# Performance work log

Hardware: AMD Instinct MI355X
Metric: run time of the kernel (lower is better)

Reference implementation:

```python
import jax, jax.numpy as jnp
import numpy as np

B, C, H, W = 4, 128, 64, 64
NUM_HEADS = 4
EPS = 1e-5


def setup_inputs() -> dict:
    key = jax.random.key(0)
    k1, k2, k3 = jax.random.split(key, 3)
    x = jax.random.normal(k1, (B, C, H, W), dtype=jnp.float32)
    gn_w = jnp.ones((C,), jnp.float32)
    gn_b = jnp.zeros((C,), jnp.float32)
    qkv_w = 0.02 * jax.random.normal(k2, (3 * C, C), dtype=jnp.float32)
    qkv_b = jnp.zeros((3 * C,), jnp.float32)
    proj_w = 0.02 * jax.random.normal(k3, (C, C), dtype=jnp.float32)
    proj_b = jnp.zeros((C,), jnp.float32)
    return {"x": x, "gn_w": gn_w, "gn_b": gn_b, "qkv_w": qkv_w,
            "qkv_b": qkv_b, "proj_w": proj_w, "proj_b": proj_b}


def reference(x, gn_w, gn_b, qkv_w, qkv_b, proj_w, proj_b):
    b, c, h, w = x.shape
    nh = NUM_HEADS
    dh = c // nh
    hw = h * w
    # GroupNorm with 1 group: normalize over (C,H,W) per sample, biased var
    mean = jnp.mean(x, axis=(1, 2, 3), keepdims=True)
    var = jnp.var(x, axis=(1, 2, 3), keepdims=True)
    xn = (x - mean) * jax.lax.rsqrt(var + EPS)
    xn = xn * gn_w[None, :, None, None] + gn_b[None, :, None, None]
    # 1x1 conv == channel matmul: (b,c,h,w) -> (b,3c,h,w)
    qkv = jnp.einsum('bchw,oc->bohw', xn, qkv_w) + qkv_b[None, :, None, None]
    qkv = qkv.reshape(b, 3, nh, dh, hw)
    q, k, v = qkv[:, 0], qkv[:, 1], qkv[:, 2]  # each (b, nh, dh, hw)
    scale = dh ** (-0.5)
    # attn: (b, nh, hw, hw)
    attn = jax.nn.softmax(jnp.einsum('bhdn,bhdm->bhnm', q, k) * scale, axis=-1)
    out = jnp.einsum('bhnm,bhdm->bhnd', attn, v)  # (b, nh, hw, dh)
    # faithful to torch: permute(0,3,1,2) -> (b, dh, nh, hw), then reshape(b,c,h,w)
    out = jnp.transpose(out, (0, 3, 1, 2)).reshape(b, c, h, w)
    out = jnp.einsum('bchw,oc->bohw', out, proj_w) + proj_b[None, :, None, None]
    return out + x
```

## Files before the change

### kernel.cpp

```cpp
#include <hip/hip_runtime.h>
#include <math.h>

#define HW 4096
#define CH 128
#define NH 4
#define DH 32

typedef unsigned short u16;
typedef __attribute__((ext_vector_type(8))) short bf16x8;
typedef __attribute__((ext_vector_type(4))) float f32x4;
typedef __attribute__((ext_vector_type(16))) float f32x16;
typedef __attribute__((ext_vector_type(4))) unsigned short u16x4;
typedef __attribute__((ext_vector_type(8))) unsigned short u16x8;

#if __has_builtin(__builtin_amdgcn_exp2f)
#define KFOLD (0.17677669529663687f * 1.4426950408889634f)
#define FASTEXP(x) __builtin_amdgcn_exp2f(x)
#else
#define KFOLD 0.17677669529663687f
#define FASTEXP(x) __expf(x)
#endif

#if __has_builtin(__builtin_amdgcn_rcpf)
#define RCPF(x) __builtin_amdgcn_rcpf(x)
#else
#define RCPF(x) (1.f / (x))
#endif

__device__ __forceinline__ u16 f2bf(float f) {
    union { float f; unsigned u; } a; a.f = f;
    unsigned u = a.u;
    unsigned r = u + 0x7FFFu + ((u >> 16) & 1u);
    return (u16)(r >> 16);
}
__device__ __forceinline__ float bf2f(u16 u) {
    union { unsigned u; float f; } a; a.u = ((unsigned)u) << 16;
    return a.f;
}
__device__ __forceinline__ unsigned pack2bf_t(float a, float b) {
    union { float f; unsigned u; } ua, ub; ua.f = a; ub.f = b;
    return __builtin_amdgcn_perm(ub.u, ua.u, 0x07060302u);
}

__global__ __launch_bounds__(256) void prep_kernel(
    const float* __restrict__ x, float* __restrict__ partials,
    const float* __restrict__ qkv_w, const float* __restrict__ proj_w,
    u16* __restrict__ wq, u16* __restrict__ wp) {
    int blk = blockIdx.x, t = threadIdx.x;
    if (blk < 512) {
        const float4* xv = (const float4*)(x + (size_t)blk * 4096);
        float s = 0.f, sq = 0.f;
#pragma unroll
        for (int i = 0; i < 4; ++i) {
            float4 v = xv[t + 256 * i];
            s  += v.x + v.y + v.z + v.w;
            sq += v.x * v.x + v.y * v.y + v.z * v.z + v.w * v.w;
        }
#pragma unroll
        for (int off = 32; off > 0; off >>= 1) {
            s  += __shfl_down(s, off, 64);
            sq += __shfl_down(sq, off, 64);
        }
        __shared__ float red[8];
        int wave = t >> 6, lane = t & 63;
        if (lane == 0) { red[wave * 2] = s; red[wave * 2 + 1] = sq; }
        __syncthreads();
        if (t == 0) {
            partials[blk * 2]     = red[0] + red[2] + red[4] + red[6];
            partials[blk * 2 + 1] = red[1] + red[3] + red[5] + red[7];
        }
    } else {
        int i = (blk - 512) * 256 + t;
        if (i < 49152) {
            int dstBlk = i >> 9, lane = (i >> 3) & 63, j = i & 7;
            int wave = dstBlk / 24, rem = dstBlk % 24;
            int os = rem >> 2, kc = rem & 3;
            int o = wave * 96 + os * 16 + (lane & 15);
            int c = kc * 32 + (lane >> 4) * 8 + j;
            wq[i] = f2bf(qkv_w[o * 128 + c]);
        } else {
            int i2 = i - 49152;
            int dstBlk = i2 >> 9, lane = (i2 >> 3) & 63, j = i2 & 7;
            int wave = dstBlk >> 3, rem = dstBlk & 7;
            int os = rem >> 2, kc = rem & 3;
            int o = wave * 32 + os * 16 + (lane & 15);
            int c = kc * 32 + (lane >> 4) * 8 + j;
            wp[i2] = f2bf(proj_w[o * 128 + c]);
        }
    }
}

__global__ __launch_bounds__(256) void qkv_mfma_kernel(
    const float* __restrict__ x, const float* __restrict__ gn_w, const float* __restrict__ gn_b,
    const u16* __restrict__ wq, const float* __restrict__ qkv_b, const float* __restrict__ partials,
    u16* __restrict__ qo, u16* __restrict__ ko, u16* __restrict__ vo) {
    __shared__ u16 xt[32 * 136];
    __shared__ float sstats[2];
    int b = blockIdx.y, p0 = blockIdx.x * 32, t = threadIdx.x;
    const float* xb = x + (size_t)b * CH * HW;
    float4 xv[4]; int cc[4], pp[4];
#pragma unroll
    for (int i = 0; i < 4; ++i) {
        int u = t + 256 * i;
        cc[i] = u >> 3; pp[i] = (u & 7) * 4;
        xv[i] = *(const float4*)&xb[(size_t)cc[i] * HW + p0 + pp[i]];
    }
    if (t < 64) {
        float s  = partials[(b * 128 + t) * 2]     + partials[(b * 128 + 64 + t) * 2];
        float sq = partials[(b * 128 + t) * 2 + 1] + partials[(b * 128 + 64 + t) * 2 + 1];
#pragma unroll
        for (int off = 32; off > 0; off >>= 1) {
            s  += __shfl_down(s, off, 64);
            sq += __shfl_down(sq, off, 64);
        }
        if (t == 0) {
            const float invN = 1.f / (float)(CH * HW);
            float mean = s * invN;
            float var  = sq * invN - mean * mean;
            sstats[0] = mean;
            sstats[1] = rsqrtf(var + 1e-5f);
        }
    }
    __syncthreads();
    float mean = sstats[0], rstd = sstats[1];
#pragma unroll
    for (int i = 0; i < 4; ++i) {
        float sc = rstd * gn_w[cc[i]], bb = gn_b[cc[i]] - mean * sc;
        xt[(pp[i] + 0) * 136 + cc[i]] = f2bf(fmaf(xv[i].x, sc, bb));
        xt[(pp[i] + 1) * 136 + cc[i]] = f2bf(fmaf(xv[i].y, sc, bb));
        xt[(pp[i] + 2) * 136 + cc[i]] = f2bf(fmaf(xv[i].z, sc, bb));
        xt[(pp[i] + 3) * 136 + cc[i]] = f2bf(fmaf(xv[i].w, sc, bb));
    }
    __syncthreads();
    int wave = t >> 6, lane = t & 63, l16 = lane & 15, quad = lane >> 4;
    f32x4 acc[6][2];
#pragma unroll
    for (int os = 0; os < 6; ++os)
#pragma unroll
        for (int ps = 0; ps < 2; ++ps) acc[os][ps] = f32x4{0.f, 0.f, 0.f, 0.f};
#pragma unroll
    for (int kc = 0; kc < 4; ++kc) {
        bf16x8 bfr[2];
#pragma unroll
        for (int ps = 0; ps < 2; ++ps)
            bfr[ps] = *(const bf16x8*)&xt[(ps * 16 + l16) * 136 + kc * 32 + quad * 8];
#pragma unroll
        for (int os = 0; os < 6; ++os) {
            bf16x8 af = *(const bf16x8*)&wq[((wave * 6 + os) * 4 + kc) * 512 + lane * 8];
#pragma unroll
            for (int ps = 0; ps < 2; ++ps)
                acc[os][ps] = __builtin_amdgcn_mfma_f32_16x16x32_bf16(af, bfr[ps], acc[os][ps], 0, 0, 0);
        }
    }
#pragma unroll
    for (int os = 0; os < 6; ++os) {
        int obase = wave * 96 + os * 16 + quad * 4;
        int sec = obase >> 7;
        if (sec == 2) continue;
        float4 bias = *(const float4*)&qkv_b[obase];
        int oc = obase & 127, h = oc >> 5, d = oc & 31;
        float km = (sec == 1) ? KFOLD : 1.f;
#pragma unroll
        for (int ps = 0; ps < 2; ++ps) {
            int p = p0 + ps * 16 + l16;
            u16x4 pk = {f2bf((acc[os][ps][0] + bias.x) * km),
                        f2bf((acc[os][ps][1] + bias.y) * km),
                        f2bf((acc[os][ps][2] + bias.z) * km),
                        f2bf((acc[os][ps][3] + bias.w) * km)};
            *(u16x4*)((sec == 0 ? qo : ko) + ((size_t)(b * NH + h) * HW + p) * DH + d) = pk;
        }
    }
    __syncthreads();
    u16* vt = xt;
    int l16p2 = (l16 & 3) | ((l16 & 4) << 1) | ((l16 & 8) >> 1);
#pragma unroll
    for (int os = 0; os < 6; ++os) {
        int obase = wave * 96 + os * 16 + quad * 4;
        if ((obase >> 7) != 2) continue;
        float4 bias = *(const float4*)&qkv_b[obase];
        int oc = obase & 127;
#pragma unroll
        for (int ps = 0; ps < 2; ++ps) {
            int colm = ps * 16 + l16p2;
            vt[(oc + 0) * 34 + colm] = f2bf(acc[os][ps][0] + bias.x);
            vt[(oc + 1) * 34 + colm] = f2bf(acc[os][ps][1] + bias.y);
            vt[(oc + 2) * 34 + colm] = f2bf(acc[os][ps][2] + bias.z);
            vt[(oc + 3) * 34 + colm] = f2bf(acc[os][ps][3] + bias.w);
        }
    }
    __syncthreads();
#pragma unroll
    for (int i = 0; i < 2; ++i) {
        int row = i * 64 + (t >> 2), colv = (t & 3) * 8;
        *(u16x8*)&vo[((size_t)b * CH + row) * HW + p0 + colv] = *(const u16x8*)&vt[row * 34 + colv];
    }
}

__global__ __launch_bounds__(256, 4) void attn_mfma_kernel(
    const u16* __restrict__ q, const u16* __restrict__ k, const u16* __restrict__ v,
    u16* __restrict__ Op, float* __restrict__ lp) {
    __shared__ u16 smem[18944];
    int bh = blockIdx.z, mpart = blockIdx.y, t = threadIdx.x;
    int wave = t >> 6, lane = t & 63, l31 = lane & 31, hf = lane >> 5;
    const u16* qb = q + (size_t)bh * HW * DH;
    const u16* kb = k + (size_t)bh * HW * DH;
    const u16* vb = v + (size_t)bh * DH * HW;
    int n_g = blockIdx.x * 128 + wave * 32 + l31;
    int m_base = mpart * 2048;

    bf16x8 bq0 = *(const bf16x8*)&qb[(size_t)n_g * DH + hf * 8];
    bf16x8 bq1 = *(const bf16x8*)&qb[(size_t)n_g * DH + 16 + hf * 8];

    int km_ = t >> 2, kg_ = t & 3;
    int kw0 = km_ * 40 + kg_ * 8, kw1 = kw0 + 64 * 40;
    const u16* kgp = kb + (size_t)(m_base + km_) * DH + kg_ * 8;
    int vd_ = t >> 3, vg_ = t & 7;
    int vw0 = vd_ * 136 + vg_ * 8, vw1 = vw0 + 64;
    const u16* vgp = vb + (size_t)vd_ * HW + m_base + vg_ * 8;

    int kro[2][2], vro[4];
#pragma unroll
    for (int ms = 0; ms < 2; ++ms)
#pragma unroll
        for (int kc = 0; kc < 2; ++kc)
            kro[ms][kc] = (ms * 32 + l31) * 40 + (2 * kc + hf) * 8;
#pragma unroll
    for (int kc = 0; kc < 4; ++kc)
        vro[kc] = l31 * 136 + (2 * kc + hf) * 8;

    const f32x16 zero16 = {0.f,0.f,0.f,0.f,0.f,0.f,0.f,0.f,0.f,0.f,0.f,0.f,0.f,0.f,0.f,0.f};
    f32x16 accO = zero16;
    float l_part = 0.f;

    bf16x8 kregA = *(const bf16x8*)kgp;
    bf16x8 kregB = *(const bf16x8*)(kgp + 64 * DH);
    bf16x8 vregA = *(const bf16x8*)vgp;
    bf16x8 vregB = *(const bf16x8*)(vgp + 64);

    for (int it = 0; it < 16; ++it) {
        u16* Ksb = smem + (it & 1) * 5120;
        u16* Vsb = smem + 10240 + (it & 1) * 4352;
        *(bf16x8*)&Ksb[kw0] = kregA;
        *(bf16x8*)&Ksb[kw1] = kregB;
        *(bf16x8*)&Vsb[vw0] = vregA;
        *(bf16x8*)&Vsb[vw1] = vregB;
        __syncthreads();
        if (it < 15) {
            const u16* kp = kgp + (size_t)(it + 1) * 128 * DH;
            kregA = *(const bf16x8*)kp;
            kregB = *(const bf16x8*)(kp + 64 * DH);
            const u16* vp = vgp + (it + 1) * 128;
            vregA = *(const bf16x8*)vp;
            vregB = *(const bf16x8*)(vp + 64);
        }
#pragma unroll
        for (int h = 0; h < 2; ++h) {
            const u16* Kh = Ksb + h * 2560;
            f32x16 s0, s1;
            {
                bf16x8 a00 = *(const bf16x8*)&Kh[kro[0][0]];
                bf16x8 a01 = *(const bf16x8*)&Kh[kro[0][1]];
                s0 = __builtin_amdgcn_mfma_f32_32x32x16_bf16(a00, bq0, zero16, 0, 0, 0);
                s0 = __builtin_amdgcn_mfma_f32_32x32x16_bf16(a01, bq1, s0, 0, 0, 0);
                bf16x8 a10 = *(const bf16x8*)&Kh[kro[1][0]];
                bf16x8 a11 = *(const bf16x8*)&Kh[kro[1][1]];
                s1 = __builtin_amdgcn_mfma_f32_32x32x16_bf16(a10, bq0, zero16, 0, 0, 0);
                s1 = __builtin_amdgcn_mfma_f32_32x32x16_bf16(a11, bq1, s1, 0, 0, 0);
            }
            unsigned pk[2][8];
#pragma unroll
            for (int qq = 0; qq < 8; ++qq) {
                float e0 = FASTEXP(s0[2 * qq]), e1 = FASTEXP(s0[2 * qq + 1]);
                l_part += e0 + e1;
                pk[0][qq] = pack2bf_t(e0, e1);
                float f0 = FASTEXP(s1[2 * qq]), f1 = FASTEXP(s1[2 * qq + 1]);
                l_part += f0 + f1;
                pk[1][qq] = pack2bf_t(f0, f1);
            }
#pragma unroll
            for (int kc = 0; kc < 4; ++kc) {
                int ms = kc >> 1, Qb = 4 * (kc & 1);
                union { unsigned u[4]; bf16x8 v; } bu;
                bu.u[0] = pk[ms][Qb + 0];
                bu.u[1] = pk[ms][Qb + 1];
                bu.u[2] = pk[ms][Qb + 2];
                bu.u[3] = pk[ms][Qb + 3];
                bf16x8 av = *(const bf16x8*)&Vsb[vro[kc] + h * 64];
                accO = __builtin_amdgcn_mfma_f32_32x32x16_bf16(av, bu.v, accO, 0, 0, 0);
            }
        }
    }
    l_part += __shfl_xor(l_part, 32, 64);
    if (hf == 0) lp[((size_t)bh * HW + n_g) * 2 + mpart] = l_part;
    __syncthreads();
    u16* tb = smem;
    int nloc = wave * 32 + l31;
#pragma unroll
    for (int r = 0; r < 16; ++r) {
        int d = (r & 3) + 8 * (r >> 2) + 4 * hf;
        tb[nloc * 40 + d] = f2bf(accO[r]);
    }
    __syncthreads();
    size_t obase = ((size_t)(mpart * 16 + bh) * HW + blockIdx.x * 128) * 32;
#pragma unroll
    for (int i = 0; i < 2; ++i) {
        int row = i * 64 + (t >> 2), col = (t & 3) * 8;
        *(u16x8*)&Op[obase + (size_t)row * 32 + col] = *(const u16x8*)&tb[row * 40 + col];
    }
}

__global__ __launch_bounds__(256) void proj_mfma_kernel(
    const u16* __restrict__ Op, const float* __restrict__ lp,
    const u16* __restrict__ wp, const float* __restrict__ proj_b,
    const float* __restrict__ x, float* __restrict__ out) {
    __shared__ u16 at_t[32 * 136];
    int b = blockIdx.y, p0 = blockIdx.x * 32, t = threadIdx.x;
#pragma unroll
    for (int i = 0; i < 2; ++i) {
        int u = t + 256 * i;
        int p = u >> 4, hh = (u >> 2) & 3, ch = u & 3;
        int bh = b * NH + hh;
        size_t nidx = (size_t)bh * HW + p0 + p;
        float2 l2 = *(const float2*)&lp[nidx * 2];
        float lsum = l2.x + l2.y;
        float sum8[8] = {0.f,0.f,0.f,0.f,0.f,0.f,0.f,0.f};
#pragma unroll
        for (int part = 0; part < 2; ++part) {
            u16x8 ov = *(const u16x8*)&Op[((size_t)(part * 16 + bh) * HW + p0 + p) * 32 + ch * 8];
#pragma unroll
            for (int j = 0; j < 8; ++j) sum8[j] += bf2f(ov[j]);
        }
        float rin = RCPF(lsum);
#pragma unroll
        for (int j = 0; j < 8; ++j)
            at_t[p * 136 + (ch * 8 + j) * 4 + hh] = f2bf(sum8[j] * rin);
    }
    __syncthreads();
    int wave = t >> 6, lane = t & 63, l16 = lane & 15, quad = lane >> 4;
    f32x4 acc[2][2];
#pragma unroll
    for (int os = 0; os < 2; ++os)
#pragma unroll
        for (int ps = 0; ps < 2; ++ps) acc[os][ps] = f32x4{0.f, 0.f, 0.f, 0.f};
#pragma unroll
    for (int kc = 0; kc < 4; ++kc) {
        bf16x8 bfr[2];
#pragma unroll
        for (int ps = 0; ps < 2; ++ps)
            bfr[ps] = *(const bf16x8*)&at_t[(ps * 16 + l16) * 136 + kc * 32 + quad * 8];
#pragma unroll
        for (int os = 0; os < 2; ++os) {
            bf16x8 af = *(const bf16x8*)&wp[((wave * 2 + os) * 4 + kc) * 512 + lane * 8];
#pragma unroll
            for (int ps = 0; ps < 2; ++ps)
                acc[os][ps] = __builtin_amdgcn_mfma_f32_16x16x32_bf16(af, bfr[ps], acc[os][ps], 0, 0, 0);
        }
    }
#pragma unroll
    for (int os = 0; os < 2; ++os) {
        int obase = wave * 32 + os * 16 + quad * 4;
#pragma unroll
        for (int ps = 0; ps < 2; ++ps) {
            int p = p0 + ps * 16 + l16;
#pragma unroll
            for (int r = 0; r < 4; ++r) {
                size_t idx = ((size_t)b * CH + obase + r) * HW + p;
                out[idx] = acc[os][ps][r] + proj_b[obase + r] + x[idx];
            }
        }
    }
}

extern "C" void kernel_launch(void* const* d_in, const int* in_sizes, int n_in,
                              void* d_out, int out_size, void* d_ws, size_t ws_size,
                              hipStream_t stream) {
    const float* x      = (const float*)d_in[0];
    const float* gn_w   = (const float*)d_in[1];
    const float* gn_b   = (const float*)d_in[2];
    const float* qkv_w  = (const float*)d_in[3];
    const float* qkv_b  = (const float*)d_in[4];
    const float* proj_w = (const float*)d_in[5];
    const float* proj_b = (const float*)d_in[6];
    float* out = (float*)d_out;

    char* W = (char*)d_ws;
    float* partials = (float*)(W + 0);
    u16*   wq       = (u16*)(W + 8192);
    u16*   wp       = (u16*)(W + 8192 + 98304);
    u16*   qo       = (u16*)(W + 139264);
    u16*   ko       = qo + (size_t)2097152;
    u16*   vo       = ko + (size_t)2097152;
    u16*   Op       = vo + (size_t)2097152;
    float* lp       = (float*)(Op + (size_t)2 * 2097152);

    hipLaunchKernelGGL(prep_kernel,      dim3(768),       dim3(256), 0, stream,
                       x, partials, qkv_w, proj_w, wq, wp);
    hipLaunchKernelGGL(qkv_mfma_kernel,  dim3(128, 4),    dim3(256), 0, stream,
                       x, gn_w, gn_b, wq, qkv_b, partials, qo, ko, vo);
    hipLaunchKernelGGL(attn_mfma_kernel, dim3(32, 2, 16), dim3(256), 0, stream,
                       qo, ko, vo, Op, lp);
    hipLaunchKernelGGL(proj_mfma_kernel, dim3(128, 4),    dim3(256), 0, stream,
                       Op, lp, wp, proj_b, x, out);
}
```

Measured before the change: 137.4 us.

## Halve pixel tile in qkv/proj kernels and split attention accumulator chain

The qkv and proj kernels now process 16 pixels per block instead of 32, doubling the grid to 1024 blocks so more work spreads across CUs, at the cost of reloading weights from global memory twice as often. The attention kernel splits its PV accumulator into two independent MFMA chains (and two row-sum partials), combined at the end, to cut the dependency stall between back-to-back 32x32 MFMAs. The extra accumulator adds 16 registers per lane, which may pressure occupancy under the launch bound of 4.

```diff
diff --git a/kernel.cpp b/kernel.cpp
--- a/kernel.cpp
+++ b/kernel.cpp
@@ -94,15 +94,15 @@
     const float* __restrict__ x, const float* __restrict__ gn_w, const float* __restrict__ gn_b,
     const u16* __restrict__ wq, const float* __restrict__ qkv_b, const float* __restrict__ partials,
     u16* __restrict__ qo, u16* __restrict__ ko, u16* __restrict__ vo) {
-    __shared__ u16 xt[32 * 136];
+    __shared__ u16 smem[3072];
     __shared__ float sstats[2];
-    int b = blockIdx.y, p0 = blockIdx.x * 32, t = threadIdx.x;
+    int b = blockIdx.y, p0 = blockIdx.x * 16, t = threadIdx.x;
     const float* xb = x + (size_t)b * CH * HW;
-    float4 xv[4]; int cc[4], pp[4];
-#pragma unroll
-    for (int i = 0; i < 4; ++i) {
+    float4 xv[2]; int cc[2], pp[2];
+#pragma unroll
+    for (int i = 0; i < 2; ++i) {
         int u = t + 256 * i;
-        cc[i] = u >> 3; pp[i] = (u & 7) * 4;
+        cc[i] = u >> 2; pp[i] = (u & 3) * 4;
         xv[i] = *(const float4*)&xb[(size_t)cc[i] * HW + p0 + pp[i]];
     }
     if (t < 64) {
@@ -123,8 +123,9 @@
     }
     __syncthreads();
     float mean = sstats[0], rstd = sstats[1];
-#pragma unroll
-    for (int i = 0; i < 4; ++i) {
+    u16* xt = smem;
+#pragma unroll
+    for (int i = 0; i < 2; ++i) {
         float sc = rstd * gn_w[cc[i]], bb = gn_b[cc[i]] - mean * sc;
         xt[(pp[i] + 0) * 136 + cc[i]] = f2bf(fmaf(xv[i].x, sc, bb));
         xt[(pp[i] + 1) * 136 + cc[i]] = f2bf(fmaf(xv[i].y, sc, bb));
@@ -133,25 +134,19 @@
     }
     __syncthreads();
     int wave = t >> 6, lane = t & 63, l16 = lane & 15, quad = lane >> 4;
-    f32x4 acc[6][2];
-#pragma unroll
-    for (int os = 0; os < 6; ++os)
-#pragma unroll
-        for (int ps = 0; ps < 2; ++ps) acc[os][ps] = f32x4{0.f, 0.f, 0.f, 0.f};
+    f32x4 acc[6];
+#pragma unroll
+    for (int os = 0; os < 6; ++os) acc[os] = f32x4{0.f, 0.f, 0.f, 0.f};
 #pragma unroll
     for (int kc = 0; kc < 4; ++kc) {
-        bf16x8 bfr[2];
-#pragma unroll
-        for (int ps = 0; ps < 2; ++ps)
-            bfr[ps] = *(const bf16x8*)&xt[(ps * 16 + l16) * 136 + kc * 32 + quad * 8];
+        bf16x8 bfr = *(const bf16x8*)&xt[l16 * 136 + kc * 32 + quad * 8];
 #pragma unroll
         for (int os = 0; os < 6; ++os) {
             bf16x8 af = *(const bf16x8*)&wq[((wave * 6 + os) * 4 + kc) * 512 + lane * 8];
-#pragma unroll
-            for (int ps = 0; ps < 2; ++ps)
-                acc[os][ps] = __builtin_amdgcn_mfma_f32_16x16x32_bf16(af, bfr[ps], acc[os][ps], 0, 0, 0);
-        }
-    }
+            acc[os] = __builtin_amdgcn_mfma_f32_16x16x32_bf16(af, bfr, acc[os], 0, 0, 0);
+        }
+    }
+    int p = p0 + l16;
 #pragma unroll
     for (int os = 0; os < 6; ++os) {
         int obase = wave * 96 + os * 16 + quad * 4;
@@ -160,18 +155,14 @@
         float4 bias = *(const float4*)&qkv_b[obase];
         int oc = obase & 127, h = oc >> 5, d = oc & 31;
         float km = (sec == 1) ? KFOLD : 1.f;
-#pragma unroll
-        for (int ps = 0; ps < 2; ++ps) {
-            int p = p0 + ps * 16 + l16;
-            u16x4 pk = {f2bf((acc[os][ps][0] + bias.x) * km),
-                        f2bf((acc[os][ps][1] + bias.y) * km),
-                        f2bf((acc[os][ps][2] + bias.z) * km),
-                        f2bf((acc[os][ps][3] + bias.w) * km)};
-            *(u16x4*)((sec == 0 ? qo : ko) + ((size_t)(b * NH + h) * HW + p) * DH + d) = pk;
-        }
-    }
-    __syncthreads();
-    u16* vt = xt;
+        u16x4 pk = {f2bf((acc[os][0] + bias.x) * km),
+                    f2bf((acc[os][1] + bias.y) * km),
+                    f2bf((acc[os][2] + bias.z) * km),
+                    f2bf((acc[os][3] + bias.w) * km)};
+        *(u16x4*)((sec == 0 ? qo : ko) + ((size_t)(b * NH + h) * HW + p) * DH + d) = pk;
+    }
+    __syncthreads();
+    u16* vt = smem;
     int l16p2 = (l16 & 3) | ((l16 & 4) << 1) | ((l16 & 8) >> 1);
 #pragma unroll
     for (int os = 0; os < 6; ++os) {
@@ -179,20 +170,15 @@
         if ((obase >> 7) != 2) continue;
         float4 bias = *(const float4*)&qkv_b[obase];
         int oc = obase & 127;
-#pragma unroll
-        for (int ps = 0; ps < 2; ++ps) {
-            int colm = ps * 16 + l16p2;
-            vt[(oc + 0) * 34 + colm] = f2bf(acc[os][ps][0] + bias.x);
-            vt[(oc + 1) * 34 + colm] = f2bf(acc[os][ps][1] + bias.y);
-            vt[(oc + 2) * 34 + colm] = f2bf(acc[os][ps][2] + bias.z);
-            vt[(oc + 3) * 34 + colm] = f2bf(acc[os][ps][3] + bias.w);
-        }
-    }
-    __syncthreads();
-#pragma unroll
-    for (int i = 0; i < 2; ++i) {
-        int row = i * 64 + (t >> 2), colv = (t & 3) * 8;
-        *(u16x8*)&vo[((size_t)b * CH + row) * HW + p0 + colv] = *(const u16x8*)&vt[row * 34 + colv];
+        vt[(oc + 0) * 24 + l16p2] = f2bf(acc[os][0] + bias.x);
+        vt[(oc + 1) * 24 + l16p2] = f2bf(acc[os][1] + bias.y);
+        vt[(oc + 2) * 24 + l16p2] = f2bf(acc[os][2] + bias.z);
+        vt[(oc + 3) * 24 + l16p2] = f2bf(acc[os][3] + bias.w);
+    }
+    __syncthreads();
+    {
+        int row = t >> 1, col = (t & 1) * 8;
+        *(u16x8*)&vo[((size_t)b * CH + row) * HW + p0 + col] = *(const u16x8*)&vt[row * 24 + col];
     }
 }
 
@@ -229,8 +215,8 @@
         vro[kc] = l31 * 136 + (2 * kc + hf) * 8;
 
     const f32x16 zero16 = {0.f,0.f,0.f,0.f,0.f,0.f,0.f,0.f,0.f,0.f,0.f,0.f,0.f,0.f,0.f,0.f};
-    f32x16 accO = zero16;
-    float l_part = 0.f;
+    f32x16 accO0 = zero16, accO1 = zero16;
+    float l0 = 0.f, l1 = 0.f;
 
     bf16x8 kregA = *(const bf16x8*)kgp;
     bf16x8 kregB = *(const bf16x8*)(kgp + 64 * DH);
@@ -271,10 +257,10 @@
 #pragma unroll
             for (int qq = 0; qq < 8; ++qq) {
                 float e0 = FASTEXP(s0[2 * qq]), e1 = FASTEXP(s0[2 * qq + 1]);
-                l_part += e0 + e1;
+                l0 += e0 + e1;
                 pk[0][qq] = pack2bf_t(e0, e1);
                 float f0 = FASTEXP(s1[2 * qq]), f1 = FASTEXP(s1[2 * qq + 1]);
-                l_part += f0 + f1;
+                l1 += f0 + f1;
                 pk[1][qq] = pack2bf_t(f0, f1);
             }
 #pragma unroll
@@ -286,10 +272,15 @@
                 bu.u[2] = pk[ms][Qb + 2];
                 bu.u[3] = pk[ms][Qb + 3];
                 bf16x8 av = *(const bf16x8*)&Vsb[vro[kc] + h * 64];
-                accO = __builtin_amdgcn_mfma_f32_32x32x16_bf16(av, bu.v, accO, 0, 0, 0);
+                if (kc < 2)
+                    accO0 = __builtin_amdgcn_mfma_f32_32x32x16_bf16(av, bu.v, accO0, 0, 0, 0);
+                else
+                    accO1 = __builtin_amdgcn_mfma_f32_32x32x16_bf16(av, bu.v, accO1, 0, 0, 0);
             }
         }
     }
+    f32x16 accO = accO0 + accO1;
+    float l_part = l0 + l1;
     l_part += __shfl_xor(l_part, 32, 64);
     if (hf == 0) lp[((size_t)bh * HW + n_g) * 2 + mpart] = l_part;
     __syncthreads();
@@ -313,12 +304,10 @@
     const u16* __restrict__ Op, const float* __restrict__ lp,
     const u16* __restrict__ wp, const float* __restrict__ proj_b,
     const float* __restrict__ x, float* __restrict__ out) {
-    __shared__ u16 at_t[32 * 136];
-    int b = blockIdx.y, p0 = blockIdx.x * 32, t = threadIdx.x;
-#pragma unroll
-    for (int i = 0; i < 2; ++i) {
-        int u = t + 256 * i;
-        int p = u >> 4, hh = (u >> 2) & 3, ch = u & 3;
+    __shared__ u16 at_t[16 * 136];
+    int b = blockIdx.y, p0 = blockIdx.x * 16, t = threadIdx.x;
+    {
+        int p = t >> 4, hh = (t >> 2) & 3, ch = t & 3;
         int bh = b * NH + hh;
         size_t nidx = (size_t)bh * HW + p0 + p;
         float2 l2 = *(const float2*)&lp[nidx * 2];
@@ -337,36 +326,26 @@
     }
     __syncthreads();
     int wave = t >> 6, lane = t & 63, l16 = lane & 15, quad = lane >> 4;
-    f32x4 acc[2][2];
-#pragma unroll
-    for (int os = 0; os < 2; ++os)
-#pragma unroll
-        for (int ps = 0; ps < 2; ++ps) acc[os][ps] = f32x4{0.f, 0.f, 0.f, 0.f};
+    f32x4 acc[2];
+    acc[0] = f32x4{0.f, 0.f, 0.f, 0.f};
+    acc[1] = f32x4{0.f, 0.f, 0.f, 0.f};
 #pragma unroll
     for (int kc = 0; kc < 4; ++kc) {
-        bf16x8 bfr[2];
-#pragma unroll
-        for (int ps = 0; ps < 2; ++ps)
-            bfr[ps] = *(const bf16x8*)&at_t[(ps * 16 + l16) * 136 + kc * 32 + quad * 8];
+        bf16x8 bfr = *(const bf16x8*)&at_t[l16 * 136 + kc * 32 + quad * 8];
 #pragma unroll
         for (int os = 0; os < 2; ++os) {
             bf16x8 af = *(const bf16x8*)&wp[((wave * 2 + os) * 4 + kc) * 512 + lane * 8];
-#pragma unroll
-            for (int ps = 0; ps < 2; ++ps)
-                acc[os][ps] = __builtin_amdgcn_mfma_f32_16x16x32_bf16(af, bfr[ps], acc[os][ps], 0, 0, 0);
-        }
-    }
+            acc[os] = __builtin_amdgcn_mfma_f32_16x16x32_bf16(af, bfr, acc[os], 0, 0, 0);
+        }
+    }
+    int p = p0 + l16;
 #pragma unroll
     for (int os = 0; os < 2; ++os) {
         int obase = wave * 32 + os * 16 + quad * 4;
 #pragma unroll
-        for (int ps = 0; ps < 2; ++ps) {
-            int p = p0 + ps * 16 + l16;
-#pragma unroll
-            for (int r = 0; r < 4; ++r) {
-                size_t idx = ((size_t)b * CH + obase + r) * HW + p;
-                out[idx] = acc[os][ps][r] + proj_b[obase + r] + x[idx];
-            }
+        for (int r = 0; r < 4; ++r) {
+            size_t idx = ((size_t)b * CH + obase + r) * HW + p;
+            out[idx] = acc[os][r] + proj_b[obase + r] + x[idx];
         }
     }
 }
@@ -395,10 +374,10 @@
 
     hipLaunchKernelGGL(prep_kernel,      dim3(768),       dim3(256), 0, stream,
                        x, partials, qkv_w, proj_w, wq, wp);
-    hipLaunchKernelGGL(qkv_mfma_kernel,  dim3(128, 4),    dim3(256), 0, stream,
+    hipLaunchKernelGGL(qkv_mfma_kernel,  dim3(256, 4),    dim3(256), 0, stream,
                        x, gn_w, gn_b, wq, qkv_b, partials, qo, ko, vo);
     hipLaunchKernelGGL(attn_mfma_kernel, dim3(32, 2, 16), dim3(256), 0, stream,
                        qo, ko, vo, Op, lp);
-    hipLaunchKernelGGL(proj_mfma_kernel, dim3(128, 4),    dim3(256), 0, stream,
+    hipLaunchKernelGGL(proj_mfma_kernel, dim3(256, 4),    dim3(256), 0, stream,
                        Op, lp, wp, proj_b, x, out);
 }
```

Result: slower. 148.2 us (+7.9%).

## Process two query tiles per wave to reuse K/V loads, split keys four ways

Applied to the files above, without the earlier changes.

Each attention block now handles 256 queries (two 32-row sub-tiles per wave) and reuses each K/V fragment read from shared memory for both, which halves K/V global and LDS traffic per query. The key dimension is split into four parts of 1024 instead of two of 2048, which keeps the grid size unchanged. The projection kernel now reduces four partial outputs and four partial sums per query. The cost is more registers (two accumulators, two sets of Q fragments, with the occupancy hint removed) and extra partial-output memory and reduction work in the projection step.

```diff
diff --git a/kernel.cpp b/kernel.cpp
--- a/kernel.cpp
+++ b/kernel.cpp
@@ -196,7 +196,7 @@
     }
 }
 
-__global__ __launch_bounds__(256, 4) void attn_mfma_kernel(
+__global__ __launch_bounds__(256) void attn_mfma_kernel(
     const u16* __restrict__ q, const u16* __restrict__ k, const u16* __restrict__ v,
     u16* __restrict__ Op, float* __restrict__ lp) {
     __shared__ u16 smem[18944];
@@ -205,11 +205,15 @@
     const u16* qb = q + (size_t)bh * HW * DH;
     const u16* kb = k + (size_t)bh * HW * DH;
     const u16* vb = v + (size_t)bh * DH * HW;
-    int n_g = blockIdx.x * 128 + wave * 32 + l31;
-    int m_base = mpart * 2048;
-
-    bf16x8 bq0 = *(const bf16x8*)&qb[(size_t)n_g * DH + hf * 8];
-    bf16x8 bq1 = *(const bf16x8*)&qb[(size_t)n_g * DH + 16 + hf * 8];
+    int n_base = blockIdx.x * 256 + wave * 32 + l31;
+    int m_base = mpart * 1024;
+
+    bf16x8 bq0[2], bq1[2];
+#pragma unroll
+    for (int s = 0; s < 2; ++s) {
+        bq0[s] = *(const bf16x8*)&qb[(size_t)(n_base + s * 128) * DH + hf * 8];
+        bq1[s] = *(const bf16x8*)&qb[(size_t)(n_base + s * 128) * DH + 16 + hf * 8];
+    }
 
     int km_ = t >> 2, kg_ = t & 3;
     int kw0 = km_ * 40 + kg_ * 8, kw1 = kw0 + 64 * 40;
@@ -229,15 +233,16 @@
         vro[kc] = l31 * 136 + (2 * kc + hf) * 8;
 
     const f32x16 zero16 = {0.f,0.f,0.f,0.f,0.f,0.f,0.f,0.f,0.f,0.f,0.f,0.f,0.f,0.f,0.f,0.f};
-    f32x16 accO = zero16;
-    float l_part = 0.f;
+    f32x16 accO[2];
+    accO[0] = zero16; accO[1] = zero16;
+    float lprt[2] = {0.f, 0.f};
 
     bf16x8 kregA = *(const bf16x8*)kgp;
     bf16x8 kregB = *(const bf16x8*)(kgp + 64 * DH);
     bf16x8 vregA = *(const bf16x8*)vgp;
     bf16x8 vregB = *(const bf16x8*)(vgp + 64);
 
-    for (int it = 0; it < 16; ++it) {
+    for (int it = 0; it < 8; ++it) {
         u16* Ksb = smem + (it & 1) * 5120;
         u16* Vsb = smem + 10240 + (it & 1) * 4352;
         *(bf16x8*)&Ksb[kw0] = kregA;
@@ -245,7 +250,7 @@
         *(bf16x8*)&Vsb[vw0] = vregA;
         *(bf16x8*)&Vsb[vw1] = vregB;
         __syncthreads();
-        if (it < 15) {
+        if (it < 7) {
             const u16* kp = kgp + (size_t)(it + 1) * 128 * DH;
             kregA = *(const bf16x8*)kp;
             kregB = *(const bf16x8*)(kp + 64 * DH);
@@ -256,54 +261,70 @@
 #pragma unroll
         for (int h = 0; h < 2; ++h) {
             const u16* Kh = Ksb + h * 2560;
-            f32x16 s0, s1;
-            {
-                bf16x8 a00 = *(const bf16x8*)&Kh[kro[0][0]];
-                bf16x8 a01 = *(const bf16x8*)&Kh[kro[0][1]];
-                s0 = __builtin_amdgcn_mfma_f32_32x32x16_bf16(a00, bq0, zero16, 0, 0, 0);
-                s0 = __builtin_amdgcn_mfma_f32_32x32x16_bf16(a01, bq1, s0, 0, 0, 0);
-                bf16x8 a10 = *(const bf16x8*)&Kh[kro[1][0]];
-                bf16x8 a11 = *(const bf16x8*)&Kh[kro[1][1]];
-                s1 = __builtin_amdgcn_mfma_f32_32x32x16_bf16(a10, bq0, zero16, 0, 0, 0);
-                s1 = __builtin_amdgcn_mfma_f32_32x32x16_bf16(a11, bq1, s1, 0, 0, 0);
-            }
-            unsigned pk[2][8];
-#pragma unroll
-            for (int qq = 0; qq < 8; ++qq) {
-                float e0 = FASTEXP(s0[2 * qq]), e1 = FASTEXP(s0[2 * qq + 1]);
-                l_part += e0 + e1;
-                pk[0][qq] = pack2bf_t(e0, e1);
-                float f0 = FASTEXP(s1[2 * qq]), f1 = FASTEXP(s1[2 * qq + 1]);
-                l_part += f0 + f1;
-                pk[1][qq] = pack2bf_t(f0, f1);
+            bf16x8 a00 = *(const bf16x8*)&Kh[kro[0][0]];
+            bf16x8 a01 = *(const bf16x8*)&Kh[kro[0][1]];
+            bf16x8 a10 = *(const bf16x8*)&Kh[kro[1][0]];
+            bf16x8 a11 = *(const bf16x8*)&Kh[kro[1][1]];
+            unsigned pk[2][2][8];
+#pragma unroll
+            for (int s = 0; s < 2; ++s) {
+                {
+                    f32x16 s0 = __builtin_amdgcn_mfma_f32_32x32x16_bf16(a00, bq0[s], zero16, 0, 0, 0);
+                    s0 = __builtin_amdgcn_mfma_f32_32x32x16_bf16(a01, bq1[s], s0, 0, 0, 0);
+#pragma unroll
+                    for (int qq = 0; qq < 8; ++qq) {
+                        float e0 = FASTEXP(s0[2 * qq]), e1 = FASTEXP(s0[2 * qq + 1]);
+                        lprt[s] += e0 + e1;
+                        pk[s][0][qq] = pack2bf_t(e0, e1);
+                    }
+                }
+                {
+                    f32x16 s1 = __builtin_amdgcn_mfma_f32_32x32x16_bf16(a10, bq0[s], zero16, 0, 0, 0);
+                    s1 = __builtin_amdgcn_mfma_f32_32x32x16_bf16(a11, bq1[s], s1, 0, 0, 0);
+#pragma unroll
+                    for (int qq = 0; qq < 8; ++qq) {
+                        float f0 = FASTEXP(s1[2 * qq]), f1 = FASTEXP(s1[2 * qq + 1]);
+                        lprt[s] += f0 + f1;
+                        pk[s][1][qq] = pack2bf_t(f0, f1);
+                    }
+                }
             }
 #pragma unroll
             for (int kc = 0; kc < 4; ++kc) {
                 int ms = kc >> 1, Qb = 4 * (kc & 1);
-                union { unsigned u[4]; bf16x8 v; } bu;
-                bu.u[0] = pk[ms][Qb + 0];
-                bu.u[1] = pk[ms][Qb + 1];
-                bu.u[2] = pk[ms][Qb + 2];
-                bu.u[3] = pk[ms][Qb + 3];
                 bf16x8 av = *(const bf16x8*)&Vsb[vro[kc] + h * 64];
-                accO = __builtin_amdgcn_mfma_f32_32x32x16_bf16(av, bu.v, accO, 0, 0, 0);
+#pragma unroll
+                for (int s = 0; s < 2; ++s) {
+                    union { unsigned u[4]; bf16x8 v; } bu;
+                    bu.u[0] = pk[s][ms][Qb + 0];
+                    bu.u[1] = pk[s][ms][Qb + 1];
+                    bu.u[2] = pk[s][ms][Qb + 2];
+                    bu.u[3] = pk[s][ms][Qb + 3];
+                    accO[s] = __builtin_amdgcn_mfma_f32_32x32x16_bf16(av, bu.v, accO[s], 0, 0, 0);
+                }
             }
         }
     }
-    l_part += __shfl_xor(l_part, 32, 64);
-    if (hf == 0) lp[((size_t)bh * HW + n_g) * 2 + mpart] = l_part;
+#pragma unroll
+    for (int s = 0; s < 2; ++s) {
+        lprt[s] += __shfl_xor(lprt[s], 32, 64);
+        if (hf == 0) lp[((size_t)bh * HW + n_base + s * 128) * 4 + mpart] = lprt[s];
+    }
     __syncthreads();
     u16* tb = smem;
-    int nloc = wave * 32 + l31;
-#pragma unroll
-    for (int r = 0; r < 16; ++r) {
-        int d = (r & 3) + 8 * (r >> 2) + 4 * hf;
-        tb[nloc * 40 + d] = f2bf(accO[r]);
-    }
-    __syncthreads();
-    size_t obase = ((size_t)(mpart * 16 + bh) * HW + blockIdx.x * 128) * 32;
-#pragma unroll
-    for (int i = 0; i < 2; ++i) {
+#pragma unroll
+    for (int s = 0; s < 2; ++s) {
+        int nloc = s * 128 + wave * 32 + l31;
+#pragma unroll
+        for (int r = 0; r < 16; ++r) {
+            int d = (r & 3) + 8 * (r >> 2) + 4 * hf;
+            tb[nloc * 40 + d] = f2bf(accO[s][r]);
+        }
+    }
+    __syncthreads();
+    size_t obase = ((size_t)(mpart * 16 + bh) * HW + blockIdx.x * 256) * 32;
+#pragma unroll
+    for (int i = 0; i < 4; ++i) {
         int row = i * 64 + (t >> 2), col = (t & 3) * 8;
         *(u16x8*)&Op[obase + (size_t)row * 32 + col] = *(const u16x8*)&tb[row * 40 + col];
     }
@@ -321,11 +342,11 @@
         int p = u >> 4, hh = (u >> 2) & 3, ch = u & 3;
         int bh = b * NH + hh;
         size_t nidx = (size_t)bh * HW + p0 + p;
-        float2 l2 = *(const float2*)&lp[nidx * 2];
-        float lsum = l2.x + l2.y;
+        float4 l4 = *(const float4*)&lp[nidx * 4];
+        float lsum = (l4.x + l4.y) + (l4.z + l4.w);
         float sum8[8] = {0.f,0.f,0.f,0.f,0.f,0.f,0.f,0.f};
 #pragma unroll
-        for (int part = 0; part < 2; ++part) {
+        for (int part = 0; part < 4; ++part) {
             u16x8 ov = *(const u16x8*)&Op[((size_t)(part * 16 + bh) * HW + p0 + p) * 32 + ch * 8];
 #pragma unroll
             for (int j = 0; j < 8; ++j) sum8[j] += bf2f(ov[j]);
@@ -391,13 +412,13 @@
     u16*   ko       = qo + (size_t)2097152;
     u16*   vo       = ko + (size_t)2097152;
     u16*   Op       = vo + (size_t)2097152;
-    float* lp       = (float*)(Op + (size_t)2 * 2097152);
+    float* lp       = (float*)(Op + (size_t)4 * 2097152);
 
     hipLaunchKernelGGL(prep_kernel,      dim3(768),       dim3(256), 0, stream,
                        x, partials, qkv_w, proj_w, wq, wp);
     hipLaunchKernelGGL(qkv_mfma_kernel,  dim3(128, 4),    dim3(256), 0, stream,
                        x, gn_w, gn_b, wq, qkv_b, partials, qo, ko, vo);
-    hipLaunchKernelGGL(attn_mfma_kernel, dim3(32, 2, 16), dim3(256), 0, stream,
+    hipLaunchKernelGGL(attn_mfma_kernel, dim3(16, 4, 16), dim3(256), 0, stream,
                        qo, ko, vo, Op, lp);
     hipLaunchKernelGGL(proj_mfma_kernel, dim3(128, 4),    dim3(256), 0, stream,
                        Op, lp, wp, proj_b, x, out);
```

Result: no change. 139.7 us (+1.6%).
